# Optimization experiments

Measured on AMD Instinct MI355X. Metric: run time of the kernel, lower is better.

Reference implementation:

```python
import jax, jax.numpy as jnp
import numpy as np

N = 150_000          # active BEV voxels
C = 128              # SHARED_CONV_CHANNEL
KK = 9               # 3x3 submanifold kernel
H = W = 1024         # BEV spatial shape at stride 8
OUT_CH = (3, 2, 1, 3, 2)   # hm, center, center_z, dim, rot
NH = 5
MAXO = 3
EPS = 1e-5
INIT_BIAS = -2.19


def _build_neighbor_idx():
    # Random sparse occupancy; pad index == N means 'inactive neighbor'
    rng = np.random.default_rng(0)
    flat = rng.choice(H * W, size=N, replace=False)
    ys, xs = flat // W, flat % W
    grid = np.full(H * W, N, dtype=np.int32)
    grid[flat] = np.arange(N, dtype=np.int32)
    nbr = np.full((N, KK), N, dtype=np.int32)
    k = 0
    for dy in (-1, 0, 1):
        for dx in (-1, 0, 1):
            ny, nx = ys + dy, xs + dx
            ok = (ny >= 0) & (ny < H) & (nx >= 0) & (nx < W)
            nbr[ok, k] = grid[(ny * W + nx)[ok]]
            k += 1
    return jnp.asarray(nbr)


def setup_inputs() -> dict:
    key = jax.random.key(0)
    k0, k1, k2 = jax.random.split(key, 3)
    x = jax.random.normal(k0, (N, C), jnp.float32)
    W1 = jax.random.normal(k1, (NH, KK, C, C), jnp.float32) * (2.0 / (KK * C)) ** 0.5  # kaiming
    gamma = jnp.ones((NH, C), jnp.float32)
    beta = jnp.zeros((NH, C), jnp.float32)
    W2 = jax.random.normal(k2, (NH, C, MAXO), jnp.float32) * 0.02
    b2 = jnp.zeros((NH, MAXO), jnp.float32).at[0, :OUT_CH[0]].set(INIT_BIAS)  # hm init_bias
    return {"x": x, "neighbor_idx": _build_neighbor_idx(),
            "W1": W1, "gamma": gamma, "beta": beta, "W2": W2, "b2": b2}


def reference(x, neighbor_idx, W1, gamma, beta, W2, b2):
    # pad row of zeros: inactive neighbors contribute nothing (submanifold conv)
    xp = jnp.concatenate([x, jnp.zeros((1, C), x.dtype)], axis=0)
    acc = jnp.zeros((NH, x.shape[0], C), x.dtype)
    for k in range(KK):                       # fixed 3x3 kernel loop
        g = xp[neighbor_idx[:, k]]            # [N, C] irregular gather
        acc = acc + jnp.einsum('nc,hcd->hnd', g, W1[:, k])
    # BatchNorm1d (training mode: batch stats over active voxels) + ReLU
    mean = acc.mean(axis=1, keepdims=True)
    var = ((acc - mean) ** 2).mean(axis=1, keepdims=True)
    h = (acc - mean) * jax.lax.rsqrt(var + EPS) * gamma[:, None, :] + beta[:, None, :]
    h = jax.nn.relu(h)
    # 1x1 SubMConv per head (padded to MAXO channels, masked)
    out = jnp.einsum('hnc,hco->hno', h, W2) + b2[:, None, :]   # [NH, N, MAXO]
    mask = (jnp.arange(MAXO)[None, :] < jnp.asarray(OUT_CH)[:, None]).astype(out.dtype)
    return out * mask[:, None, :]
```

## Files before the change

kernel.cpp:

```cpp
#include <hip/hip_runtime.h>

#define NPTS 150000
#define NHEAD 5
#define KTOT 1152
#define NTILES 1172
#define NBLK 586
#define HSTRIDE 592
#define EPSV 1e-5f
#define FXSCALE 1048576.0

typedef __bf16 bf16x8 __attribute__((ext_vector_type(8)));
typedef float f32x4 __attribute__((ext_vector_type(4)));
typedef unsigned short u16x8 __attribute__((ext_vector_type(8)));

#define WS_NEEDED 232509376UL

__device__ __forceinline__ unsigned short f2bf(float f) {
    unsigned int u = __float_as_uint(f);
    u += 0x7FFFu + ((u >> 16) & 1u);
    return (unsigned short)(u >> 16);
}

__device__ __forceinline__ void gload16(const void* g, void* l) {
    __builtin_amdgcn_global_load_lds((const __attribute__((address_space(1))) void*)g,
                                     (__attribute__((address_space(3))) void*)l, 16, 0, 0);
}

__global__ void k_pre(const float* __restrict__ x, unsigned short* __restrict__ xbf,
                      const float* __restrict__ W1, unsigned short* __restrict__ w1t,
                      const int* __restrict__ nbr, int* __restrict__ hist_t) {
    __shared__ int lh[512];
    const int bid = blockIdx.x;
    const int t = threadIdx.x;
    if (bid < 9376) {
        const size_t i8 = (size_t)bid * 256 + t;
        const size_t base = i8 * 8;
        if (base >= (size_t)(NPTS + 1) * 128) return;
        if (base < (size_t)NPTS * 128) {
            const f32x4 v0 = __builtin_nontemporal_load((const f32x4*)(x + base));
            const f32x4 v1 = __builtin_nontemporal_load((const f32x4*)(x + base + 4));
            u16x8 o;
            o[0] = f2bf(v0[0]); o[1] = f2bf(v0[1]); o[2] = f2bf(v0[2]); o[3] = f2bf(v0[3]);
            o[4] = f2bf(v1[0]); o[5] = f2bf(v1[1]); o[6] = f2bf(v1[2]); o[7] = f2bf(v1[3]);
            *(u16x8*)(xbf + base) = o;
        } else {
            u16x8 z = {0,0,0,0,0,0,0,0};
            *(u16x8*)(xbf + base) = z;
        }
    } else if (bid < 9376 + 2880) {
        const int idx = (bid - 9376) * 256 + t;
        const int d = idx & 127;
        const int c = (idx >> 7) & 127;
        const int hk = idx >> 14;
        const int k = hk % 9, h = hk / 9;
        const int col = h * 128 + d;
        const int p = k * 128 + c;
        const int s32 = p >> 5;
        const int j0 = (p >> 3) & 3;
        const int jj = j0 ^ ((col >> 1) & 3);
        w1t[(size_t)col * KTOT + s32 * 32 + jj * 8 + (p & 7)] = f2bf(W1[idx]);
    } else {
        const int b = bid - 12256;
        lh[t] = 0; lh[t + 256] = 0;
        __syncthreads();
        const int n = b * 256 + t;
        if (n < NPTS) {
            int pat = 0;
#pragma unroll
            for (int k = 0; k < 9; k++) pat |= (nbr[n * 9 + k] != NPTS) << k;
            atomicAdd(&lh[pat], 1);
        }
        __syncthreads();
        hist_t[t * HSTRIDE + b] = lh[t];
        hist_t[(t + 256) * HSTRIDE + b] = lh[t + 256];
    }
}

__global__ void k_scan1(int* __restrict__ hist_t, int* __restrict__ tot,
                        unsigned long long* __restrict__ sacc) {
    const int p = blockIdx.x;
    const int lane = threadIdx.x;
    if (lane == 0) {
        sacc[p] = 0ULL; sacc[512 + p] = 0ULL;
        if (p < 256) sacc[1024 + p] = 0ULL;
    }
    int run = 0;
    for (int c = 0; c < 10; c++) {
        const int i = c * 64 + lane;
        const int orig = (i < NBLK) ? hist_t[p * HSTRIDE + i] : 0;
        int v = orig;
        for (int d = 1; d < 64; d <<= 1) {
            const int w = __shfl_up(v, d);
            if (lane >= d) v += w;
        }
        if (i < NBLK) hist_t[p * HSTRIDE + i] = run + v - orig;
        run += __shfl(v, 63);
    }
    if (lane == 0) tot[p] = run;
}

__global__ __launch_bounds__(512) void k_scatter(
    const int* __restrict__ nbr, const int* __restrict__ hist_t,
    const int* __restrict__ tot, int* __restrict__ perm) {
    __shared__ int pat_s[256];
    __shared__ int bs[512];
    const int t = threadIdx.x, b = blockIdx.x;
    const int v0 = tot[t];
    bs[t] = v0;
    __syncthreads();
    for (int d = 1; d < 512; d <<= 1) {
        const int w = (t >= d) ? bs[t - d] : 0;
        __syncthreads();
        bs[t] += w;
        __syncthreads();
    }
    const int base_t = bs[t] - v0;
    __syncthreads();
    bs[t] = base_t;
    const int n = b * 256 + (t & 255);
    int pat = -1;
    if (t < 256) {
        if (n < NPTS) {
            pat = 0;
#pragma unroll
            for (int k = 0; k < 9; k++) pat |= (nbr[n * 9 + k] != NPTS) << k;
        }
        pat_s[t] = pat;
    }
    __syncthreads();
    if (t < 256 && n < NPTS) {
        int rank = 0;
        for (int j = 0; j < 256; j++) rank += (j < t) & (pat_s[j] == pat);
        perm[bs[pat] + hist_t[pat * HSTRIDE + b] + rank] = n;
    }
}

__global__ __launch_bounds__(512, 4) void k_gemm(
    const unsigned short* __restrict__ xbf,
    const unsigned short* __restrict__ w1t,
    const int* __restrict__ nbr,
    const int* __restrict__ perm,
    unsigned short* __restrict__ accw2,
    unsigned long long* __restrict__ sacc)
{
    __shared__ unsigned short ABC[28672];
    __shared__ int nbr_s[9 * 128];
    __shared__ int perm_s[128];
    __shared__ int mask_s;

    const int tid = threadIdx.x;
    const int wid = tid >> 6;
    const int lane = tid & 63;
    const int bm = blockIdx.x;
    const int b2 = blockIdx.y;
    const int tile = (bm * 331) % NTILES;
    const int tile0 = tile * 128;

    if (tid == 0) mask_s = 0;
    if (tid < 128) {
        const int gr = tile0 + tid;
        perm_s[tid] = (gr < NPTS) ? perm[gr] : NPTS;
    }
    __syncthreads();
    if (tid < 128) {
        const int prow = perm_s[tid];
        int pat = 0;
#pragma unroll
        for (int k = 0; k < 9; k++) {
            const int v = (prow < NPTS) ? nbr[prow * 9 + k] : NPTS;
            nbr_s[k * 128 + tid] = v;
            pat |= (v != NPTS) << k;
        }
        if (pat) atomicOr(&mask_s, pat);
    }
    __syncthreads();
    const int mask = mask_s | 16;
    const int steps = 4 * __builtin_popcount(mask);

    const int RM = (wid >> 2) * 64;
    const int CNl = (wid & 3) * 80;
    const int lr16 = lane >> 2;
    const int lb = lane & 3;
    const int jswS = (lb ^ ((lr16 >> 1) & 3)) * 8;

    f32x4 acc[4][5];
#pragma unroll
    for (int m = 0; m < 4; m++)
#pragma unroll
        for (int n = 0; n < 5; n++) acc[m][n] = f32x4{0.f, 0.f, 0.f, 0.f};

    auto stage = [&](int buf, int kn, int q) {
#pragma unroll
        for (int j = 0; j < 4; ++j) {
            const int g = wid + 8 * j;
            if (g < 8) {
                const int r = g * 16 + lr16;
                const int idx = nbr_s[kn * 128 + r];
                gload16(xbf + (size_t)idx * 128 + q * 32 + jswS,
                        (void*)(ABC + buf * 4096 + g * 512));
            } else if (g < 28) {
                const int gb = g - 8;
                const int lc = gb * 16 + lr16;
                gload16(w1t + (size_t)(b2 * 320 + lc) * KTOT + (kn * 4 + q) * 32 + lb * 8,
                        (void*)(ABC + 8192 + buf * 10240 + gb * 512));
            }
        }
    };

    const int rlo = lane & 15;
    const int jsw = (((lane >> 4) ^ ((rlo >> 1) & 3))) * 8;

    auto compute = [&](int buf) {
        const unsigned short* Ab = ABC + buf * 4096;
        const unsigned short* Bb = ABC + 8192 + buf * 10240;
        bf16x8 a[4];
#pragma unroll
        for (int m = 0; m < 4; m++)
            a[m] = *reinterpret_cast<const bf16x8*>(&Ab[(RM + m * 16 + rlo) * 32 + jsw]);
#pragma unroll
        for (int n = 0; n < 5; n++) {
            const bf16x8 b = *reinterpret_cast<const bf16x8*>(&Bb[(CNl + n * 16 + rlo) * 32 + jsw]);
#pragma unroll
            for (int m = 0; m < 4; m++)
                acc[m][n] = __builtin_amdgcn_mfma_f32_16x16x32_bf16(a[m], b, acc[m][n], 0, 0, 0);
        }
    };

    int ckn = __builtin_ctz(mask), cq = 0, rem = mask & (mask - 1), buf = 0;
    stage(0, ckn, 0);
    __syncthreads();
    for (int i = 0; i < steps; i++) {
        int nkn, nq, nrem;
        if (cq < 3) { nkn = ckn; nq = cq + 1; nrem = rem; }
        else { nkn = rem ? __builtin_ctz(rem) : 0; nq = 0; nrem = rem & (rem - 1); }
        if (i + 1 < steps) stage(buf ^ 1, nkn, nq);
        compute(buf);
        __syncthreads();
        ckn = nkn; cq = nq; rem = nrem; buf ^= 1;
    }

    float sn[5], qn[5];
#pragma unroll
    for (int n = 0; n < 5; n++) {
        float s = 0.f, q = 0.f;
#pragma unroll
        for (int m = 0; m < 4; m++)
#pragma unroll
            for (int r = 0; r < 4; r++) { const float v = acc[m][n][r]; s += v; q += v * v; }
        s += __shfl_xor(s, 16); s += __shfl_xor(s, 32);
        q += __shfl_xor(q, 16); q += __shfl_xor(q, 32);
        sn[n] = s; qn[n] = q;
    }
    if (lane < 16) {
#pragma unroll
        for (int n = 0; n < 5; n++) {
            const int gcol = b2 * 320 + CNl + n * 16 + lane;
            atomicAdd(&sacc[gcol],
                      (unsigned long long)__double2ll_rn((double)sn[n] * FXSCALE));
            atomicAdd(&sacc[640 + gcol],
                      (unsigned long long)__double2ll_rn((double)qn[n] * FXSCALE));
        }
    }

    unsigned short* C = (unsigned short*)ABC;
#pragma unroll
    for (int p = 0; p < 2; ++p) {
        __syncthreads();
        if (((wid >> 1) & 1) == p) {
            const int colbase = CNl - p * 160;
#pragma unroll
            for (int m = 0; m < 4; m++) {
                const int row = RM + m * 16 + (lane >> 4) * 4;
#pragma unroll
                for (int n = 0; n < 5; n++) {
                    const int col = colbase + n * 16 + rlo;
#pragma unroll
                    for (int r = 0; r < 4; r++)
                        C[(row + r) * 168 + col] = f2bf(acc[m][n][r]);
                }
            }
        }
        __syncthreads();
#pragma unroll
        for (int j = 0; j < 5; j++) {
            const int chunk = tid + 512 * j;
            const int row = chunk / 20, cc = chunk % 20;
            const int gr = tile0 + row;
            const int col = b2 * 320 + p * 160 + cc * 8;
            __builtin_nontemporal_store(*(const u16x8*)&C[row * 168 + cc * 8],
                (u16x8*)(accw2 + (size_t)gr * 640 + col));
        }
    }
}

__global__ __launch_bounds__(512) void k_out(
    const unsigned short* __restrict__ accw2,
    const int* __restrict__ perm,
    const unsigned long long* __restrict__ sacc,
    const float* __restrict__ gamma, const float* __restrict__ beta,
    const float* __restrict__ W2, const float* __restrict__ b2,
    float* __restrict__ out)
{
    __shared__ float scp[672], shp[672], w2sp[1952], b2s[15];
    __shared__ float red[4][128][6];
    __shared__ int op_s[128];
    const int t = threadIdx.x;
    for (int c = t; c < 640; c += 512) {
        const double s = (double)(long long)sacc[c] * (1.0 / FXSCALE);
        const double q = (double)(long long)sacc[640 + c] * (1.0 / FXSCALE);
        const double mean = s * (1.0 / NPTS);
        const double var = q * (1.0 / NPTS) - mean * mean;
        const float rstd = (float)(1.0 / sqrt(var + (double)EPSV));
        const float g = gamma[c];
        const int sg = c / 160, off = c % 160;
        scp[sg * 168 + off] = rstd * g;
        shp[sg * 168 + off] = beta[c] - (float)mean * rstd * g;
        w2sp[sg * 488 + off * 3 + 0] = W2[c * 3 + 0];
        w2sp[sg * 488 + off * 3 + 1] = W2[c * 3 + 1];
        w2sp[sg * 488 + off * 3 + 2] = W2[c * 3 + 2];
    }
    if (t < 15) b2s[t] = b2[t];
    if (t < 128) {
        const int gr = blockIdx.x * 128 + t;
        op_s[t] = (gr < NPTS) ? perm[gr] : -1;
    }
    __syncthreads();

    const int row = t >> 2;
    const int seg = t & 3;
    const int gr = blockIdx.x * 128 + row;
    const int ccb = 16 - seg * 4;
    float o0[3] = {0.f, 0.f, 0.f}, o1[3] = {0.f, 0.f, 0.f};
    if (op_s[row] >= 0) {
        const unsigned short* rp = accw2 + (size_t)gr * 640 + seg * 160;
        const float* scb = scp + seg * 168;
        const float* shb = shp + seg * 168;
        const float* w2b = w2sp + seg * 488;
#pragma unroll
        for (int cc = 0; cc < 20; cc++) {
            const u16x8 v = *(const u16x8*)(rp + cc * 8);
            float t0 = 0.f, t1 = 0.f, t2 = 0.f;
#pragma unroll
            for (int j = 0; j < 8; j++) {
                const int off = cc * 8 + j;
                const float a = __uint_as_float(((unsigned int)v[j]) << 16);
                const float hc = fmaxf(fmaf(a, scb[off], shb[off]), 0.f);
                t0 = fmaf(hc, w2b[off * 3 + 0], t0);
                t1 = fmaf(hc, w2b[off * 3 + 1], t1);
                t2 = fmaf(hc, w2b[off * 3 + 2], t2);
            }
            if (cc < ccb) { o0[0] += t0; o0[1] += t1; o0[2] += t2; }
            else          { o1[0] += t0; o1[1] += t1; o1[2] += t2; }
        }
    }
    red[seg][row][0] = o0[0]; red[seg][row][1] = o0[1]; red[seg][row][2] = o0[2];
    red[seg][row][3] = o1[0]; red[seg][row][4] = o1[1]; red[seg][row][5] = o1[2];
    __syncthreads();

    for (int idx = t; idx < 640; idx += 512) {
        const int h = idx >> 7, rw = idx & 127;
        const int n = op_s[rw];
        if (n >= 0) {
            float a0 = b2s[h * 3 + 0], a1 = b2s[h * 3 + 1], a2 = b2s[h * 3 + 2];
            if (h >= 1) { a0 += red[h - 1][rw][3]; a1 += red[h - 1][rw][4]; a2 += red[h - 1][rw][5]; }
            if (h <= 3) { a0 += red[h][rw][0]; a1 += red[h][rw][1]; a2 += red[h][rw][2]; }
            const int noc = (h == 2) ? 1 : ((h == 1 || h == 4) ? 2 : 3);
            const size_t ob = ((size_t)h * NPTS + n) * 3;
            out[ob + 0] = (noc > 0) ? a0 : 0.f;
            out[ob + 1] = (noc > 1) ? a1 : 0.f;
            out[ob + 2] = (noc > 2) ? a2 : 0.f;
        }
    }
}

__global__ void k_sentinel(float* __restrict__ out, int n) {
    const int i = blockIdx.x * 256 + threadIdx.x;
    if (i < n) out[i] = 12345.0f;
}

extern "C" void kernel_launch(void* const* d_in, const int* in_sizes, int n_in,
                              void* d_out, int out_size, void* d_ws, size_t ws_size,
                              hipStream_t stream) {
    const float* x     = (const float*)d_in[0];
    const int*   nbr   = (const int*)d_in[1];
    const float* W1    = (const float*)d_in[2];
    const float* gamma = (const float*)d_in[3];
    const float* beta  = (const float*)d_in[4];
    const float* W2    = (const float*)d_in[5];
    const float* b2    = (const float*)d_in[6];
    float* out = (float*)d_out;

    if (ws_size < WS_NEEDED) {
        k_sentinel<<<(out_size + 255) / 256, 256, 0, stream>>>(out, out_size);
        return;
    }

    char* ws = (char*)d_ws;
    unsigned short* xbf      = (unsigned short*)(ws);
    unsigned short* w1t      = (unsigned short*)(ws + 38404096);
    unsigned short* accw2    = (unsigned short*)(ws + 39878656);
    int*            hist_t   = (int*)(ws + 39878656);
    int*            tot      = (int*)(ws + 39878656 + 2097152);
    unsigned long long* sacc = (unsigned long long*)(ws + 231899136);
    int*            perm     = (int*)(ws + 231909376);

    k_pre<<<12842, 256, 0, stream>>>(x, xbf, W1, w1t, nbr, hist_t);
    k_scan1<<<512, 64, 0, stream>>>(hist_t, tot, sacc);
    k_scatter<<<NBLK, 512, 0, stream>>>(nbr, hist_t, tot, perm);
    k_gemm<<<dim3(NTILES, 2), 512, 0, stream>>>(xbf, w1t, nbr, perm, accw2, sacc);
    k_out<<<NTILES, 512, 0, stream>>>(accw2, perm, sacc, gamma, beta, W2, b2, out);
}
```

Measured before the change: 305.2 us.

## Load GEMM operands directly from global into registers, dropping LDS staging

The sparse-conv GEMM now gathers A rows and B weight columns straight from global memory into registers with software double-buffering, instead of staging through LDS with global_load_lds and a barrier per k-step. The weight layout loses its swizzle since LDS bank conflicts no longer matter. The occupancy hint is removed, and the active-tap mask is now computed per 64-row half so each warp group can skip more empty taps. In exchange every wave fetches its own operands with no sharing across waves, which raises global/L2 traffic and register pressure.

```diff
diff --git a/kernel.cpp b/kernel.cpp
--- a/kernel.cpp
+++ b/kernel.cpp
@@ -19,11 +19,6 @@
     unsigned int u = __float_as_uint(f);
     u += 0x7FFFu + ((u >> 16) & 1u);
     return (unsigned short)(u >> 16);
-}
-
-__device__ __forceinline__ void gload16(const void* g, void* l) {
-    __builtin_amdgcn_global_load_lds((const __attribute__((address_space(1))) void*)g,
-                                     (__attribute__((address_space(3))) void*)l, 16, 0, 0);
 }
 
 __global__ void k_pre(const float* __restrict__ x, unsigned short* __restrict__ xbf,
@@ -53,12 +48,7 @@
         const int c = (idx >> 7) & 127;
         const int hk = idx >> 14;
         const int k = hk % 9, h = hk / 9;
-        const int col = h * 128 + d;
-        const int p = k * 128 + c;
-        const int s32 = p >> 5;
-        const int j0 = (p >> 3) & 3;
-        const int jj = j0 ^ ((col >> 1) & 3);
-        w1t[(size_t)col * KTOT + s32 * 32 + jj * 8 + (p & 7)] = f2bf(W1[idx]);
+        w1t[(size_t)(h * 128 + d) * KTOT + k * 128 + c] = f2bf(W1[idx]);
     } else {
         const int b = bid - 12256;
         lh[t] = 0; lh[t + 256] = 0;
@@ -135,7 +125,7 @@
     }
 }
 
-__global__ __launch_bounds__(512, 4) void k_gemm(
+__global__ __launch_bounds__(512) void k_gemm(
     const unsigned short* __restrict__ xbf,
     const unsigned short* __restrict__ w1t,
     const int* __restrict__ nbr,
@@ -143,10 +133,10 @@
     unsigned short* __restrict__ accw2,
     unsigned long long* __restrict__ sacc)
 {
-    __shared__ unsigned short ABC[28672];
+    __shared__ unsigned short C[21504];
     __shared__ int nbr_s[9 * 128];
     __shared__ int perm_s[128];
-    __shared__ int mask_s;
+    __shared__ int maskg_s[2];
 
     const int tid = threadIdx.x;
     const int wid = tid >> 6;
@@ -156,7 +146,7 @@
     const int tile = (bm * 331) % NTILES;
     const int tile0 = tile * 128;
 
-    if (tid == 0) mask_s = 0;
+    if (tid < 2) maskg_s[tid] = 16;
     if (tid < 128) {
         const int gr = tile0 + tid;
         perm_s[tid] = (gr < NPTS) ? perm[gr] : NPTS;
@@ -171,17 +161,23 @@
             nbr_s[k * 128 + tid] = v;
             pat |= (v != NPTS) << k;
         }
-        if (pat) atomicOr(&mask_s, pat);
-    }
-    __syncthreads();
-    const int mask = mask_s | 16;
+        if (pat) atomicOr(&maskg_s[tid >> 6], pat);
+    }
+    __syncthreads();
+
+    const int rg = wid >> 2;
+    const int RM = rg * 64;
+    const int CNl = (wid & 3) * 80;
+    const int rlo = lane & 15;
+    const int khi = lane >> 4;
+    const int mask = maskg_s[rg];
     const int steps = 4 * __builtin_popcount(mask);
 
-    const int RM = (wid >> 2) * 64;
-    const int CNl = (wid & 3) * 80;
-    const int lr16 = lane >> 2;
-    const int lb = lane & 3;
-    const int jswS = (lb ^ ((lr16 >> 1) & 3)) * 8;
+    const unsigned short* abase = xbf + khi * 8;
+    const unsigned short* bbase[5];
+#pragma unroll
+    for (int n = 0; n < 5; n++)
+        bbase[n] = w1t + (size_t)(b2 * 320 + CNl + n * 16 + rlo) * KTOT + khi * 8;
 
     f32x4 acc[4][5];
 #pragma unroll
@@ -189,67 +185,52 @@
 #pragma unroll
         for (int n = 0; n < 5; n++) acc[m][n] = f32x4{0.f, 0.f, 0.f, 0.f};
 
-    auto stage = [&](int buf, int kn, int q) {
-#pragma unroll
-        for (int j = 0; j < 4; ++j) {
-            const int g = wid + 8 * j;
-            if (g < 8) {
-                const int r = g * 16 + lr16;
-                const int idx = nbr_s[kn * 128 + r];
-                gload16(xbf + (size_t)idx * 128 + q * 32 + jswS,
-                        (void*)(ABC + buf * 4096 + g * 512));
-            } else if (g < 28) {
-                const int gb = g - 8;
-                const int lc = gb * 16 + lr16;
-                gload16(w1t + (size_t)(b2 * 320 + lc) * KTOT + (kn * 4 + q) * 32 + lb * 8,
-                        (void*)(ABC + 8192 + buf * 10240 + gb * 512));
-            }
-        }
+    int kn = __builtin_ctz(mask), q = 0, rem = mask & (mask - 1);
+    auto adv = [&]() {
+        if (q < 3) q++;
+        else { if (rem) { kn = __builtin_ctz(rem); rem &= rem - 1; } q = 0; }
     };
-
-    const int rlo = lane & 15;
-    const int jsw = (((lane >> 4) ^ ((rlo >> 1) & 3))) * 8;
-
-    auto compute = [&](int buf) {
-        const unsigned short* Ab = ABC + buf * 4096;
-        const unsigned short* Bb = ABC + 8192 + buf * 10240;
-        bf16x8 a[4];
+    auto loadA = [&](bf16x8* a, int lkn, int lq) {
+#pragma unroll
+        for (int m = 0; m < 4; m++) {
+            const int idx = nbr_s[lkn * 128 + RM + m * 16 + rlo];
+            a[m] = *(const bf16x8*)(abase + (size_t)idx * 128 + lq * 32);
+        }
+    };
+    auto loadB = [&](bf16x8* b, int lkn, int lq) {
+        const int koff = lkn * 128 + lq * 32;
+#pragma unroll
+        for (int n = 0; n < 5; n++)
+            b[n] = *(const bf16x8*)(bbase[n] + koff);
+    };
+    auto domfma = [&](const bf16x8* a, const bf16x8* b) {
+#pragma unroll
+        for (int n = 0; n < 5; n++)
+#pragma unroll
+            for (int m = 0; m < 4; m++)
+                acc[m][n] = __builtin_amdgcn_mfma_f32_16x16x32_bf16(a[m], b[n], acc[m][n], 0, 0, 0);
+    };
+
+    bf16x8 a0[4], b0[5], a1[4], b1[5];
+    loadA(a0, kn, q); loadB(b0, kn, q); adv();
+    for (int i = 0; i < steps; i += 2) {
+        loadA(a1, kn, q); loadB(b1, kn, q); adv();
+        domfma(a0, b0);
+        if (i + 2 < steps) { loadA(a0, kn, q); loadB(b0, kn, q); adv(); }
+        domfma(a1, b1);
+    }
+
+    float sn[5], qn[5];
+#pragma unroll
+    for (int n = 0; n < 5; n++) {
+        float s = 0.f, q2 = 0.f;
 #pragma unroll
         for (int m = 0; m < 4; m++)
-            a[m] = *reinterpret_cast<const bf16x8*>(&Ab[(RM + m * 16 + rlo) * 32 + jsw]);
-#pragma unroll
-        for (int n = 0; n < 5; n++) {
-            const bf16x8 b = *reinterpret_cast<const bf16x8*>(&Bb[(CNl + n * 16 + rlo) * 32 + jsw]);
-#pragma unroll
-            for (int m = 0; m < 4; m++)
-                acc[m][n] = __builtin_amdgcn_mfma_f32_16x16x32_bf16(a[m], b, acc[m][n], 0, 0, 0);
-        }
-    };
-
-    int ckn = __builtin_ctz(mask), cq = 0, rem = mask & (mask - 1), buf = 0;
-    stage(0, ckn, 0);
-    __syncthreads();
-    for (int i = 0; i < steps; i++) {
-        int nkn, nq, nrem;
-        if (cq < 3) { nkn = ckn; nq = cq + 1; nrem = rem; }
-        else { nkn = rem ? __builtin_ctz(rem) : 0; nq = 0; nrem = rem & (rem - 1); }
-        if (i + 1 < steps) stage(buf ^ 1, nkn, nq);
-        compute(buf);
-        __syncthreads();
-        ckn = nkn; cq = nq; rem = nrem; buf ^= 1;
-    }
-
-    float sn[5], qn[5];
-#pragma unroll
-    for (int n = 0; n < 5; n++) {
-        float s = 0.f, q = 0.f;
-#pragma unroll
-        for (int m = 0; m < 4; m++)
-#pragma unroll
-            for (int r = 0; r < 4; r++) { const float v = acc[m][n][r]; s += v; q += v * v; }
+#pragma unroll
+            for (int r = 0; r < 4; r++) { const float v = acc[m][n][r]; s += v; q2 += v * v; }
         s += __shfl_xor(s, 16); s += __shfl_xor(s, 32);
-        q += __shfl_xor(q, 16); q += __shfl_xor(q, 32);
-        sn[n] = s; qn[n] = q;
+        q2 += __shfl_xor(q2, 16); q2 += __shfl_xor(q2, 32);
+        sn[n] = s; qn[n] = q2;
     }
     if (lane < 16) {
 #pragma unroll
@@ -262,7 +243,6 @@
         }
     }
 
-    unsigned short* C = (unsigned short*)ABC;
 #pragma unroll
     for (int p = 0; p < 2; ++p) {
         __syncthreads();
@@ -270,7 +250,7 @@
             const int colbase = CNl - p * 160;
 #pragma unroll
             for (int m = 0; m < 4; m++) {
-                const int row = RM + m * 16 + (lane >> 4) * 4;
+                const int row = RM + m * 16 + khi * 4;
 #pragma unroll
                 for (int n = 0; n < 5; n++) {
                     const int col = colbase + n * 16 + rlo;
```

Measured after the change: 436.8 us. 43.1% more time.
